# Kernel tuning notes

Hardware: AMD Instinct MI355X
Metric: run time of the kernel (lower is better)

Reference implementation:

```python
import jax, jax.numpy as jnp
import numpy as np

C, N, L = 2048, 4, 16

def setup_inputs() -> dict:
    key = jax.random.key(0)
    k1, k2 = jax.random.split(key)
    tensor = jax.random.normal(k1, (C, N, L), dtype=jnp.float32)
    bias = jax.random.normal(k2, (C, N, L), dtype=jnp.float32)
    return {"tensor": tensor, "bias": bias}

def reference(tensor, bias):
    # tensor, bias: (C, N, L). Output: (C, L, L, ..., L) with N L-dims.
    tb = tensor + bias  # (C, N, L)
    # Sequential outer product across the N factor vectors, fully
    # vectorized over channels C. acc: (C, L^k) after step k.
    acc = tb[:, 0]  # (C, L)
    for n in range(1, N):
        acc = (acc[:, :, None] * tb[:, n][:, None, :]).reshape(acc.shape[0], -1)
    return acc.reshape((tensor.shape[0],) + (L,) * N)
```

## Files before the change

### kernel.cpp

```cpp
#include <hip/hip_runtime.h>


#define NC 2048
#define NL 16

typedef float f4 __attribute__((ext_vector_type(4)));

__global__ __launch_bounds__(256) void
tpe_kernel(const float* __restrict__ tensor,
           const float* __restrict__ bias,
           float* __restrict__ out) {
    __shared__ float tb[64];
    const int c = blockIdx.x;
    const int t = threadIdx.x;

    if (t < 64) {
        tb[t] = tensor[c * 64 + t] + bias[c * 64 + t];
    }
    __syncthreads();

    const int k  = (t >> 2) & 15;
    const int lq = (t & 3) * 4;
    const float ck = tb[32 + k];
    f4 v;
    v.x = ck * tb[48 + lq + 0];
    v.y = ck * tb[48 + lq + 1];
    v.z = ck * tb[48 + lq + 2];
    v.w = ck * tb[48 + lq + 3];

    float* op = out + (size_t)c * 65536;
    const int wg = t >> 6;

    #pragma unroll
    for (int s = 0; s < 64; ++s) {
        const int i = s >> 2;
        const int j = (s * 4 + wg) & 15;
        const float ab = tb[i] * tb[16 + j];
        f4 o;
        o.x = ab * v.x;
        o.y = ab * v.y;
        o.z = ab * v.z;
        o.w = ab * v.w;
        __builtin_nontemporal_store(o, (f4*)(op + s * 1024 + t * 4));
    }
}

extern "C" void kernel_launch(void* const* d_in, const int* in_sizes, int n_in,
                              void* d_out, int out_size, void* d_ws, size_t ws_size,
                              hipStream_t stream) {
    const float* tensor = (const float*)d_in[0];
    const float* bias   = (const float*)d_in[1];
    float* out = (float*)d_out;
    tpe_kernel<<<NC, 256, 0, stream>>>(tensor, bias, out);
}
```

Before: 514.5 us.

## Replace per-channel blocks with grid-wide strided sweep over contiguous output stripes

```diff
diff --git a/kernel.cpp b/kernel.cpp
--- a/kernel.cpp
+++ b/kernel.cpp
@@ -1,47 +1,46 @@
 #include <hip/hip_runtime.h>
 
 
-#define NC 2048
-#define NL 16
+#define NTHREADS 524288
+#define NITER    64
 
 typedef float f4 __attribute__((ext_vector_type(4)));
 
 __global__ __launch_bounds__(256) void
-tpe_kernel(const float* __restrict__ tensor,
-           const float* __restrict__ bias,
-           float* __restrict__ out) {
-    __shared__ float tb[64];
-    const int c = blockIdx.x;
-    const int t = threadIdx.x;
+tpe_sweep(const float* __restrict__ tensor,
+          const float* __restrict__ bias,
+          float* __restrict__ out) {
+    const int tid = blockIdx.x * 256 + threadIdx.x;
 
-    if (t < 64) {
-        tb[t] = tensor[c * 64 + t] + bias[c * 64 + t];
-    }
-    __syncthreads();
+    const int c0 = tid >> 14;
+    const int w  = (tid & 16383) * 4;
+    const int i  = w >> 12;
+    const int j  = (w >> 8) & 15;
+    const int k  = (w >> 4) & 15;
+    const int lq = w & 15;
 
-    const int k  = (t >> 2) & 15;
-    const int lq = (t & 3) * 4;
-    const float ck = tb[32 + k];
-    f4 v;
-    v.x = ck * tb[48 + lq + 0];
-    v.y = ck * tb[48 + lq + 1];
-    v.z = ck * tb[48 + lq + 2];
-    v.w = ck * tb[48 + lq + 3];
+    const float* tp = tensor + c0 * 64;
+    const float* bp = bias   + c0 * 64;
+    f4* op = (f4*)out + tid;
 
-    float* op = out + (size_t)c * 65536;
-    const int wg = t >> 6;
+    #pragma unroll 4
+    for (int n = 0; n < NITER; ++n) {
+        const float a  = tp[i]      + bp[i];
+        const float b  = tp[16 + j] + bp[16 + j];
+        const float ck = tp[32 + k] + bp[32 + k];
+        const f4 t4 = *(const f4*)(tp + 48 + lq);
+        const f4 b4 = *(const f4*)(bp + 48 + lq);
 
-    #pragma unroll
-    for (int s = 0; s < 64; ++s) {
-        const int i = s >> 2;
-        const int j = (s * 4 + wg) & 15;
-        const float ab = tb[i] * tb[16 + j];
+        const float abc = a * b * ck;
         f4 o;
-        o.x = ab * v.x;
-        o.y = ab * v.y;
-        o.z = ab * v.z;
-        o.w = ab * v.w;
-        __builtin_nontemporal_store(o, (f4*)(op + s * 1024 + t * 4));
+        o.x = abc * (t4.x + b4.x);
+        o.y = abc * (t4.y + b4.y);
+        o.z = abc * (t4.z + b4.z);
+        o.w = abc * (t4.w + b4.w);
+        *op = o;
+
+        tp += 2048; bp += 2048;
+        op += NTHREADS;
     }
 }
 
@@ -51,5 +50,5 @@
     const float* tensor = (const float*)d_in[0];
     const float* bias   = (const float*)d_in[1];
     float* out = (float*)d_out;
-    tpe_kernel<<<NC, 256, 0, stream>>>(tensor, bias, out);
+    tpe_sweep<<<NTHREADS / 256, 256, 0, stream>>>(tensor, bias, out);
 }
```

Measured after the change: 583.2 us. +13.4%, slower.
